# Kernel optimization log

Hardware: AMD Instinct MI355X
Metric: run time of the kernel (lower is better)

Reference implementation:

```python
import jax, jax.numpy as jnp
import numpy as np

N = 100000
E = 1600000
F_IN, HID, OUT = 64, 64, 32

def setup_inputs() -> dict:
    key = jax.random.key(0)
    ks = jax.random.split(key, 16)
    s = 0.05
    return {
        "x": jax.random.normal(ks[0], (N, F_IN), jnp.float32),
        "edge_index": jax.random.randint(ks[1], (2, E), 0, N, jnp.int64),
        "edge_attr": jax.random.uniform(ks[2], (E, 1), jnp.float32),
        # distance_processor: Linear(1,16) -> ReLU -> Linear(16,1)
        "Wd1": jax.random.normal(ks[3], (1, 16), jnp.float32) * s,
        "bd1": jnp.zeros((16,), jnp.float32),
        "Wd2": jax.random.normal(ks[4], (16, 1), jnp.float32) * s,
        "bd2": jnp.zeros((1,), jnp.float32),
        # conv1 / conv2 GCN linear weights (in, out) + post-aggregation bias
        "W1c": jax.random.normal(ks[5], (F_IN, HID), jnp.float32) * s,
        "b1c": jnp.zeros((HID,), jnp.float32),
        "W2c": jax.random.normal(ks[6], (HID, HID), jnp.float32) * s,
        "b2c": jnp.zeros((HID,), jnp.float32),
        # output head Linear(hidden, output)
        "Wo": jax.random.normal(ks[7], (HID, OUT), jnp.float32) * s,
        "bo": jnp.zeros((OUT,), jnp.float32),
    }


def _gcn_conv(x, src, dst, ew, W, b, n_nodes):
    """PyG GCNConv with edge weights: add self-loops (weight 1), symmetric norm."""
    h = x @ W                                            # [N, out]
    loop = jnp.arange(n_nodes, dtype=src.dtype)
    src_a = jnp.concatenate([src, loop])                 # [E+N]
    dst_a = jnp.concatenate([dst, loop])
    ew_a = jnp.concatenate([ew, jnp.ones((n_nodes,), ew.dtype)])
    deg = jax.ops.segment_sum(ew_a, dst_a, num_segments=n_nodes)
    dinv = jnp.where(deg > 0, jax.lax.rsqrt(jnp.maximum(deg, 1e-30)), 0.0)
    norm = dinv[src_a] * ew_a * dinv[dst_a]              # [E+N]
    msg = norm[:, None] * h[src_a]                       # gather + scale
    agg = jax.ops.segment_sum(msg, dst_a, num_segments=n_nodes)  # scatter-add
    return agg + b


def reference(x, edge_index, edge_attr, Wd1, bd1, Wd2, bd2, W1c, b1c, W2c, b2c, Wo, bo):
    src, dst = edge_index[0], edge_index[1]
    # edge weight from tiny MLP on distance, squeezed to [E]
    hmlp = jax.nn.relu(edge_attr @ Wd1 + bd1)
    ew = jax.nn.sigmoid(hmlp @ Wd2 + bd2)[:, 0]
    h = jax.nn.relu(_gcn_conv(x, src, dst, ew, W1c, b1c, N))
    # dropout is identity in eval mode
    h = _gcn_conv(h, src, dst, ew, W2c, b2c, N)
    return h @ Wo + bo
```

## Files before the change

kernel.cpp:

```cpp
#include <hip/hip_runtime.h>
#include <hip/hip_fp16.h>
#include <math.h>

#define NBMAX 400
#define GBUILD 512

typedef __attribute__((ext_vector_type(8))) ushort us8;

__device__ inline ushort f2bf(float f) {
    unsigned u = __float_as_uint(f);
    u += 0x7fff + ((u >> 16) & 1);
    return (ushort)(u >> 16);
}
__device__ inline float bf2f(ushort u) {
    return __uint_as_float(((unsigned)u) << 16);
}

__global__ __launch_bounds__(256) void k_tobf16(const float4* __restrict__ X4,
                                                ushort4* __restrict__ Y4, int n4) {
    int i = blockIdx.x * 256 + threadIdx.x;
    if (i >= n4) return;
    float4 v = X4[i];
    ushort4 o;
    o.x = f2bf(v.x); o.y = f2bf(v.y); o.z = f2bf(v.z); o.w = f2bf(v.w);
    Y4[i] = o;
}

__global__ __launch_bounds__(256) void k_hist(const int* __restrict__ dstv,
                                              int* __restrict__ bh,
                                              int E, int chunk) {
    __shared__ int lh[NBMAX];
    int tid = threadIdx.x;
    for (int i = tid; i < NBMAX; i += 256) lh[i] = 0;
    __syncthreads();
    int start = blockIdx.x * chunk;
    int end = min(E, start + chunk);
    for (int e = start + tid; e < end; e += 256)
        atomicAdd(&lh[dstv[e] >> 8], 1);
    __syncthreads();
    int* row = bh + (size_t)blockIdx.x * NBMAX;
    for (int i = tid; i < NBMAX; i += 256) row[i] = lh[i];
}

__global__ __launch_bounds__(256) void k_scanA(const int* __restrict__ bh,
                                               int* __restrict__ boff,
                                               int* __restrict__ btot) {
    __shared__ int s[GBUILD];
    int b = blockIdx.x;
    int t = threadIdx.x;
    int i0 = t, i1 = t + 256;
    s[i0] = bh[(size_t)i0 * NBMAX + b];
    s[i1] = bh[(size_t)i1 * NBMAX + b];
    __syncthreads();
    int c0 = s[i0], c1 = s[i1];
    for (int o = 1; o < GBUILD; o <<= 1) {
        int v0 = (i0 >= o) ? s[i0 - o] : 0;
        int v1 = (i1 >= o) ? s[i1 - o] : 0;
        __syncthreads();
        s[i0] += v0;
        s[i1] += v1;
        __syncthreads();
    }
    boff[(size_t)i0 * NBMAX + b] = s[i0] - c0;
    boff[(size_t)i1 * NBMAX + b] = s[i1] - c1;
    if (t == 0) btot[b] = s[GBUILD - 1];
}

__global__ __launch_bounds__(512) void k_scanB(const int* __restrict__ btot,
                                               int* __restrict__ bbase, int nb) {
    __shared__ int s[512];
    int t = threadIdx.x;
    int c = (t < nb) ? btot[t] : 0;
    s[t] = c;
    __syncthreads();
    for (int o = 1; o < 512; o <<= 1) {
        int v = (t >= o) ? s[t - o] : 0;
        __syncthreads();
        s[t] += v;
        __syncthreads();
    }
    if (t < nb) bbase[t] = s[t] - c;
}

__global__ __launch_bounds__(256) void k_edge_scatter(const float* __restrict__ ea,
                                                      const float* __restrict__ Wd1,
                                                      const float* __restrict__ bd1,
                                                      const float* __restrict__ Wd2,
                                                      const float* __restrict__ bd2,
                                                      const int* __restrict__ srcv,
                                                      const int* __restrict__ dstv,
                                                      const int* __restrict__ bbase,
                                                      const int* __restrict__ boff,
                                                      int2* __restrict__ spk,
                                                      int E, int chunk) {
    __shared__ float w1[16], b1[16], w2[16];
    __shared__ float b2s;
    __shared__ int gb[NBMAX], lc[NBMAX];
    int tid = threadIdx.x;
    if (tid < 16) {
        w1[tid] = Wd1[tid];
        b1[tid] = bd1[tid];
        w2[tid] = Wd2[tid];
    }
    if (tid == 0) b2s = bd2[0];
    const int* brow = boff + (size_t)blockIdx.x * NBMAX;
    for (int i = tid; i < NBMAX; i += 256) {
        gb[i] = bbase[i] + brow[i];
        lc[i] = 0;
    }
    __syncthreads();
    int start = blockIdx.x * chunk;
    int end = min(E, start + chunk);
    for (int e = start + tid; e < end; e += 256) {
        float a = ea[e];
        float s = b2s;
#pragma unroll
        for (int j = 0; j < 16; ++j) {
            float h = fmaxf(a * w1[j] + b1[j], 0.0f);
            s += h * w2[j];
        }
        float w = 1.0f / (1.0f + expf(-s));
        int d = dstv[e];
        int b = d >> 8;
        int p = gb[b] + atomicAdd(&lc[b], 1);
        unsigned payload = ((unsigned)(d & 255) << 16) |
                           (unsigned)__half_as_ushort(__float2half(w));
        spk[p] = make_int2(srcv[e], (int)payload);
    }
}

__global__ __launch_bounds__(256) void k_group(const int2* __restrict__ spk,
                                               const int* __restrict__ bbase,
                                               int2* __restrict__ slots,
                                               int* __restrict__ rowst,
                                               int* __restrict__ cntg,
                                               float* __restrict__ dinv,
                                               int nb, int n, int E) {
    __shared__ int cnt[256], sc[256], ls[256], cur[256];
    __shared__ float dsum[256];
    int b = blockIdx.x;
    int tid = threadIdx.x;
    int r0 = bbase[b];
    int r1 = (b + 1 < nb) ? bbase[b + 1] : E;
    cnt[tid] = 0; cur[tid] = 0; dsum[tid] = 0.0f;
    __syncthreads();
    for (int i = r0 + tid; i < r1; i += 256) {
        int2 pr = spk[i];
        int dl = (pr.y >> 16) & 255;
        atomicAdd(&cnt[dl], 1);
        atomicAdd(&dsum[dl], __half2float(__ushort_as_half((ushort)(pr.y & 0xffff))));
    }
    __syncthreads();
    sc[tid] = cnt[tid];
    __syncthreads();
    for (int o = 1; o < 256; o <<= 1) {
        int v = (tid >= o) ? sc[tid - o] : 0;
        __syncthreads();
        sc[tid] += v;
        __syncthreads();
    }
    ls[tid] = sc[tid] - cnt[tid];
    int dst = (b << 8) + tid;
    if (dst < n) {
        rowst[dst] = r0 + ls[tid];
        cntg[dst] = cnt[tid];
        dinv[dst] = 1.0f / sqrtf(1.0f + dsum[tid]);
    }
    __syncthreads();
    for (int i = r0 + tid; i < r1; i += 256) {
        int2 pr = spk[i];
        int dl = (pr.y >> 16) & 255;
        float wf = __half2float(__ushort_as_half((ushort)(pr.y & 0xffff)));
        int p = r0 + ls[dl] + atomicAdd(&cur[dl], 1);
        slots[p] = make_int2(pr.x, __float_as_int(wf));
    }
}

template <int OUTC, bool RELU, bool BF16OUT>
__global__ __launch_bounds__(512) void k_agg_gemm(const ushort* __restrict__ Hb,
                                                  const int2* __restrict__ slots,
                                                  const int* __restrict__ cnt,
                                                  const int* __restrict__ rowst,
                                                  const float* __restrict__ dinv,
                                                  const float* __restrict__ W,
                                                  const float* __restrict__ bias,
                                                  void* __restrict__ Yv, int n) {
    __shared__ __align__(16) float xs[64][68];
    __shared__ __align__(16) float ws_[64 * OUTC];
    const us8* H8 = (const us8*)Hb;
    int tid = threadIdx.x;
    for (int i = tid; i < 64 * OUTC / 4; i += 512)
        ((float4*)ws_)[i] = ((const float4*)W)[i];

    int lane = tid & 63;
    int g = lane >> 3;
    int s = lane & 7;
    int gbase = lane & 56;
    int nl = (tid >> 6) * 8 + g;
    int node = blockIdx.x * 64 + nl;
    bool valid = node < n;
    int nc = valid ? node : 0;
    float di = dinv[nc];
    int c = valid ? cnt[nc] : 0;
    size_t base = (size_t)rowst[nc];

    float acc[8];
    us8 h0 = H8[(size_t)nc * 8 + s];
#pragma unroll
    for (int j = 0; j < 8; ++j) acc[j] = di * bf2f(h0[j]);

    for (int bb = 0; bb < c; bb += 8) {
        int myc = 0;
        float myw = 0.0f;
        if (bb + s < c) {
            int2 pr = slots[base + bb + s];
            myc = pr.x;
            myw = __int_as_float(pr.y) * dinv[myc];
        }
#pragma unroll
        for (int i = 0; i < 8; ++i) {
            int ni = __shfl(myc, gbase + i);
            float wi = __shfl(myw, gbase + i);
            us8 v = H8[(size_t)ni * 8 + s];
#pragma unroll
            for (int j = 0; j < 8; ++j) acc[j] += wi * bf2f(v[j]);
        }
    }
#pragma unroll
    for (int j = 0; j < 8; ++j) xs[nl][s * 8 + j] = di * acc[j];
    __syncthreads();

    int col = tid % OUTC;
    constexpr int RSLOTS = 512 / OUTC;
    constexpr int RPT = 64 / RSLOTS;
    int rs = tid / OUTC;
    float wc[64];
#pragma unroll
    for (int k = 0; k < 64; ++k) wc[k] = ws_[k * OUTC + col];
    float bcol = bias[col];

    for (int rr = 0; rr < RPT; ++rr) {
        int r = rs * RPT + rr;
        const float4* x4 = (const float4*)&xs[r][0];
        float a = 0.0f;
#pragma unroll
        for (int k4 = 0; k4 < 16; ++k4) {
            float4 v = x4[k4];
            a += v.x * wc[4 * k4 + 0];
            a += v.y * wc[4 * k4 + 1];
            a += v.z * wc[4 * k4 + 2];
            a += v.w * wc[4 * k4 + 3];
        }
        float o = a + bcol;
        if (RELU) o = fmaxf(o, 0.0f);
        int gr = blockIdx.x * 64 + r;
        if (gr < n) {
            if (BF16OUT) ((ushort*)Yv)[(size_t)gr * OUTC + col] = f2bf(o);
            else         ((float*)Yv)[(size_t)gr * OUTC + col] = o;
        }
    }
}

__global__ __launch_bounds__(256) void k_prepW(const float* __restrict__ W2c,
                                               const float* __restrict__ Wo,
                                               const float* __restrict__ b2c,
                                               const float* __restrict__ bo,
                                               float* __restrict__ W2o,
                                               float* __restrict__ bo2) {
    int t = threadIdx.x;
    for (int idx = t; idx < 64 * 32; idx += 256) {
        int i = idx >> 5, j = idx & 31;
        float s = 0.0f;
        for (int k = 0; k < 64; ++k) s += W2c[i * 64 + k] * Wo[k * 32 + j];
        W2o[idx] = s;
    }
    if (t < 32) {
        float s = bo[t];
        for (int k = 0; k < 64; ++k) s += b2c[k] * Wo[k * 32 + t];
        bo2[t] = s;
    }
}

__global__ __launch_bounds__(256) void k_edge2(const float* __restrict__ ea,
                                               const float* __restrict__ Wd1,
                                               const float* __restrict__ bd1,
                                               const float* __restrict__ Wd2,
                                               const float* __restrict__ bd2,
                                               const int* __restrict__ dstv,
                                               float* __restrict__ ew,
                                               int* __restrict__ cnt, int E) {
    __shared__ float w1[16], b1[16], w2[16];
    __shared__ float b2s;
    if (threadIdx.x < 16) {
        w1[threadIdx.x] = Wd1[threadIdx.x];
        b1[threadIdx.x] = bd1[threadIdx.x];
        w2[threadIdx.x] = Wd2[threadIdx.x];
    }
    if (threadIdx.x == 0) b2s = bd2[0];
    __syncthreads();
    int e = blockIdx.x * 256 + threadIdx.x;
    if (e >= E) return;
    float a = ea[e];
    float s = b2s;
#pragma unroll
    for (int j = 0; j < 16; ++j) {
        float h = fmaxf(a * w1[j] + b1[j], 0.0f);
        s += h * w2[j];
    }
    float w = 1.0f / (1.0f + expf(-s));
    ew[e] = w;
    atomicAdd(&cnt[dstv[e]], 1);
}

__global__ __launch_bounds__(256) void k_scan(const int* __restrict__ cnt,
                                              int* __restrict__ rowst,
                                              int* __restrict__ cursor,
                                              int* __restrict__ gcnt, int n) {
    int i = blockIdx.x * 256 + threadIdx.x;
    int lane = threadIdx.x & 63;
    int c = (i < n) ? cnt[i] : 0;
    int pref = c;
#pragma unroll
    for (int o = 1; o < 64; o <<= 1) {
        int t = __shfl_up(pref, o);
        if (lane >= o) pref += t;
    }
    int total = __shfl(pref, 63);
    int base = 0;
    if (lane == 63 && total > 0) base = atomicAdd(gcnt, total);
    base = __shfl(base, 63);
    if (i < n) {
        int start = base + pref - c;
        rowst[i] = start;
        cursor[i] = start;
    }
}

__global__ __launch_bounds__(256) void k_fill2(const int* __restrict__ srcv,
                                               const int* __restrict__ dstv,
                                               const float* __restrict__ ew,
                                               int* __restrict__ cursor,
                                               int2* __restrict__ slots, int E) {
    int e = blockIdx.x * 256 + threadIdx.x;
    if (e >= E) return;
    int p = atomicAdd(&cursor[dstv[e]], 1);
    slots[p] = make_int2(srcv[e], __float_as_int(ew[e]));
}

__global__ __launch_bounds__(256) void k_deg(const int2* __restrict__ slots,
                                             const int* __restrict__ cnt,
                                             const int* __restrict__ rowst,
                                             float* __restrict__ dinv, int n) {
    int t = blockIdx.x * 256 + threadIdx.x;
    int g = t >> 3;
    int sub = t & 7;
    if (g >= n) return;
    int c = cnt[g];
    size_t base = (size_t)rowst[g];
    float s = 0.0f;
    for (int j = sub; j < c; j += 8) s += __int_as_float(slots[base + j].y);
    s += __shfl_xor(s, 1);
    s += __shfl_xor(s, 2);
    s += __shfl_xor(s, 4);
    if (sub == 0) dinv[g] = 1.0f / sqrtf(1.0f + s);
}

extern "C" void kernel_launch(void* const* d_in, const int* in_sizes, int n_in,
                              void* d_out, int out_size, void* d_ws, size_t ws_size,
                              hipStream_t stream) {
    const float* x   = (const float*)d_in[0];
    const int*   ei  = (const int*)d_in[1];
    const float* ea  = (const float*)d_in[2];
    const float* Wd1 = (const float*)d_in[3];
    const float* bd1 = (const float*)d_in[4];
    const float* Wd2 = (const float*)d_in[5];
    const float* bd2 = (const float*)d_in[6];
    const float* W1c = (const float*)d_in[7];
    const float* b1c = (const float*)d_in[8];
    const float* W2c = (const float*)d_in[9];
    const float* b2c = (const float*)d_in[10];
    const float* Wo  = (const float*)d_in[11];
    const float* bo  = (const float*)d_in[12];

    const int N = in_sizes[0] / 64;
    const int E = in_sizes[2];
    const int* srcv = ei;
    const int* dstv = ei + E;
    const int NB = (N + 255) >> 8;

    size_t off = 0;
    auto alloc = [&](size_t bytes) -> void* {
        void* p = (char*)d_ws + off;
        off += (bytes + 255) & ~(size_t)255;
        return p;
    };

    int*    cntg  = (int*)   alloc((size_t)N * 4);
    int*    rowst = (int*)   alloc((size_t)N * 4);
    float*  dinv  = (float*) alloc((size_t)N * 4);
    ushort* xb    = (ushort*)alloc((size_t)N * 64 * 2);
    ushort* h1b   = (ushort*)alloc((size_t)N * 64 * 2);
    float*  W2o   = (float*) alloc(64 * 32 * 4);
    float*  bo2   = (float*) alloc(32 * 4);
    int2*   slots = (int2*)  alloc((size_t)E * 8);

    const int BF = (N + 63) / 64;
    const int BT = (N * 16 + 255) / 256;
    const int GB = GBUILD;
    const int CHUNK = (E + GB - 1) / GB;

    size_t base_need = off;
    size_t sort_need = base_need + (((size_t)E * 8 + 255) & ~(size_t)255)
                       + 2 * ((size_t)GB * NBMAX * 4 + 256) + 16384;
    const bool fast = ws_size >= sort_need;

    if (fast) {
        int2* spk  = (int2*)alloc((size_t)E * 8);
        int* bh    = (int*) alloc((size_t)GB * NBMAX * 4);
        int* boff  = (int*) alloc((size_t)GB * NBMAX * 4);
        int* btot  = (int*) alloc(NBMAX * 4);
        int* bbase = (int*) alloc(NBMAX * 4);

        k_tobf16<<<BT, 256, 0, stream>>>((const float4*)x, (ushort4*)xb, N * 16);
        k_hist<<<GB, 256, 0, stream>>>(dstv, bh, E, CHUNK);
        k_scanA<<<NBMAX, 256, 0, stream>>>(bh, boff, btot);
        k_scanB<<<1, 512, 0, stream>>>(btot, bbase, NB);
        k_edge_scatter<<<GB, 256, 0, stream>>>(ea, Wd1, bd1, Wd2, bd2, srcv, dstv,
                                               bbase, boff, spk, E, CHUNK);
        k_group<<<NB, 256, 0, stream>>>(spk, bbase, slots, rowst, cntg, dinv,
                                        NB, N, E);
        k_prepW<<<1, 256, 0, stream>>>(W2c, Wo, b2c, bo, W2o, bo2);
        k_agg_gemm<64, true, true><<<BF, 512, 0, stream>>>(
            xb, slots, cntg, rowst, dinv, W1c, b1c, h1b, N);
        k_agg_gemm<32, false, false><<<BF, 512, 0, stream>>>(
            h1b, slots, cntg, rowst, dinv, W2o, bo2, d_out, N);
    } else {
        float* ew   = (float*)alloc((size_t)E * 4);
        int* cursor = (int*)  alloc((size_t)N * 4);
        int* gcnt   = (int*)  alloc(256);
        const int BN = (N + 255) / 256;
        const int BE = (E + 255) / 256;
        const int BD = (N * 8 + 255) / 256;
        hipMemsetAsync(cntg, 0, (size_t)N * 4, stream);
        hipMemsetAsync(gcnt, 0, 4, stream);
        k_tobf16<<<BT, 256, 0, stream>>>((const float4*)x, (ushort4*)xb, N * 16);
        k_edge2<<<BE, 256, 0, stream>>>(ea, Wd1, bd1, Wd2, bd2, dstv, ew, cntg, E);
        k_scan<<<BN, 256, 0, stream>>>(cntg, rowst, cursor, gcnt, N);
        k_fill2<<<BE, 256, 0, stream>>>(srcv, dstv, ew, cursor, slots, E);
        k_deg<<<BD, 256, 0, stream>>>(slots, cntg, rowst, dinv, N);
        k_prepW<<<1, 256, 0, stream>>>(W2c, Wo, b2c, bo, W2o, bo2);
        k_agg_gemm<64, true, true><<<BF, 512, 0, stream>>>(
            xb, slots, cntg, rowst, dinv, W1c, b1c, h1b, N);
        k_agg_gemm<32, false, false><<<BF, 512, 0, stream>>>(
            h1b, slots, cntg, rowst, dinv, W2o, bo2, d_out, N);
    }
}
```

Before: 290.2 us.

## Enlarge build grid, cache bucket edges in LDS, prefetch aggregation slots

Raises the histogram build grid to 2048 blocks and rewrites the column scan so each thread sums 8 entries serially before a 256-wide block scan. The grouping kernel stages each bucket's packed edges in shared memory (up to 5120 entries), so the second pass reads LDS instead of global memory. The aggregation loop prefetches the next batch of slot entries one iteration ahead to hide load latency. The larger LDS cache may lower occupancy of the grouping kernel, and buckets above the cap fall back to global reads.

```diff
diff --git a/kernel.cpp b/kernel.cpp
--- a/kernel.cpp
+++ b/kernel.cpp
@@ -3,7 +3,8 @@
 #include <math.h>
 
 #define NBMAX 400
-#define GBUILD 512
+#define GBUILD 2048
+#define GCAP 5120
 
 typedef __attribute__((ext_vector_type(8))) ushort us8;
 
@@ -45,25 +46,31 @@
 __global__ __launch_bounds__(256) void k_scanA(const int* __restrict__ bh,
                                                int* __restrict__ boff,
                                                int* __restrict__ btot) {
-    __shared__ int s[GBUILD];
+    __shared__ int s[256];
     int b = blockIdx.x;
     int t = threadIdx.x;
-    int i0 = t, i1 = t + 256;
-    s[i0] = bh[(size_t)i0 * NBMAX + b];
-    s[i1] = bh[(size_t)i1 * NBMAX + b];
-    __syncthreads();
-    int c0 = s[i0], c1 = s[i1];
-    for (int o = 1; o < GBUILD; o <<= 1) {
-        int v0 = (i0 >= o) ? s[i0 - o] : 0;
-        int v1 = (i1 >= o) ? s[i1 - o] : 0;
-        __syncthreads();
-        s[i0] += v0;
-        s[i1] += v1;
-        __syncthreads();
-    }
-    boff[(size_t)i0 * NBMAX + b] = s[i0] - c0;
-    boff[(size_t)i1 * NBMAX + b] = s[i1] - c1;
-    if (t == 0) btot[b] = s[GBUILD - 1];
+    int v[8];
+    int sum = 0;
+#pragma unroll
+    for (int j = 0; j < 8; ++j) {
+        v[j] = bh[(size_t)(t * 8 + j) * NBMAX + b];
+        sum += v[j];
+    }
+    s[t] = sum;
+    __syncthreads();
+    for (int o = 1; o < 256; o <<= 1) {
+        int tv = (t >= o) ? s[t - o] : 0;
+        __syncthreads();
+        s[t] += tv;
+        __syncthreads();
+    }
+    int excl = s[t] - sum;
+#pragma unroll
+    for (int j = 0; j < 8; ++j) {
+        boff[(size_t)(t * 8 + j) * NBMAX + b] = excl;
+        excl += v[j];
+    }
+    if (t == 255) btot[b] = s[255];
 }
 
 __global__ __launch_bounds__(512) void k_scanB(const int* __restrict__ btot,
@@ -138,14 +145,19 @@
                                                int nb, int n, int E) {
     __shared__ int cnt[256], sc[256], ls[256], cur[256];
     __shared__ float dsum[256];
+    __shared__ int2 cache[GCAP];
     int b = blockIdx.x;
     int tid = threadIdx.x;
     int r0 = bbase[b];
     int r1 = (b + 1 < nb) ? bbase[b + 1] : E;
+    int m = r1 - r0;
+    bool lds = (m <= GCAP);
     cnt[tid] = 0; cur[tid] = 0; dsum[tid] = 0.0f;
-    __syncthreads();
-    for (int i = r0 + tid; i < r1; i += 256) {
-        int2 pr = spk[i];
+    if (lds)
+        for (int i = tid; i < m; i += 256) cache[i] = spk[r0 + i];
+    __syncthreads();
+    for (int i = tid; i < m; i += 256) {
+        int2 pr = lds ? cache[i] : spk[r0 + i];
         int dl = (pr.y >> 16) & 255;
         atomicAdd(&cnt[dl], 1);
         atomicAdd(&dsum[dl], __half2float(__ushort_as_half((ushort)(pr.y & 0xffff))));
@@ -167,8 +179,8 @@
         dinv[dst] = 1.0f / sqrtf(1.0f + dsum[tid]);
     }
     __syncthreads();
-    for (int i = r0 + tid; i < r1; i += 256) {
-        int2 pr = spk[i];
+    for (int i = tid; i < m; i += 256) {
+        int2 pr = lds ? cache[i] : spk[r0 + i];
         int dl = (pr.y >> 16) & 255;
         float wf = __half2float(__ushort_as_half((ushort)(pr.y & 0xffff)));
         int p = r0 + ls[dl] + atomicAdd(&cur[dl], 1);
@@ -209,14 +221,16 @@
 #pragma unroll
     for (int j = 0; j < 8; ++j) acc[j] = di * bf2f(h0[j]);
 
+    int2 pr = make_int2(0, 0);
+    if (s < c) pr = slots[base + s];
     for (int bb = 0; bb < c; bb += 8) {
         int myc = 0;
         float myw = 0.0f;
         if (bb + s < c) {
-            int2 pr = slots[base + bb + s];
             myc = pr.x;
             myw = __int_as_float(pr.y) * dinv[myc];
         }
+        if (bb + 8 + s < c) pr = slots[base + bb + 8 + s];
 #pragma unroll
         for (int i = 0; i < 8; ++i) {
             int ni = __shfl(myc, gbase + i);
```

Result: slower. 297.1 us (+2.4%).
